# Kernel tuning notes

Measured on AMD Instinct MI355X. Metric: run time of the kernel, lower is better.

## Reference

```python
import jax, jax.numpy as jnp
import numpy as np


def _gcn_conv(x, src, dst, deg_inv_sqrt, W, b):
    # PyG GCNConv: h = x @ W; out = sum_{j->i} norm_ij * h_j  (+ bias)
    # src/dst already include self-loops; deg_inv_sqrt computed with self-loops.
    h = x @ W                                   # [N, F_out]
    norm = deg_inv_sqrt[src] * deg_inv_sqrt[dst]  # [E']
    msgs = h[src] * norm[:, None]               # [E', F_out] gather + scale
    out = jax.ops.segment_sum(msgs, dst, num_segments=x.shape[0])
    return out + b


def setup_inputs() -> dict:
    key = jax.random.key(0)
    k1, k2, k3, k4, k5 = jax.random.split(key, 5)
    N, E = 100000, 3200000
    in_c, hid, out_c = 256, 32, 128
    x = jax.random.normal(k1, (N, in_c), dtype=jnp.float32)
    edge_index = jax.random.randint(k2, (2, E), 0, N, dtype=jnp.int64)
    # Glorot-init weights, zero bias (PyG GCNConv defaults)
    W1 = jax.random.normal(k3, (in_c, hid), dtype=jnp.float32) * (2.0 / (in_c + hid)) ** 0.5
    b1 = jnp.zeros((hid,), dtype=jnp.float32)
    W2 = jax.random.normal(k4, (hid, out_c), dtype=jnp.float32) * (2.0 / (hid + out_c)) ** 0.5
    b2 = jnp.zeros((out_c,), dtype=jnp.float32)
    return {"x": x, "edge_index": edge_index, "W1": W1, "b1": b1, "W2": W2, "b2": b2}


def reference(x, edge_index, W1, b1, W2, b2):
    N = x.shape[0]
    # Add self-loops once; shared by both layers.
    loop = jnp.arange(N, dtype=edge_index.dtype)
    src = jnp.concatenate([edge_index[0], loop])
    dst = jnp.concatenate([edge_index[1], loop])
    deg = jax.ops.segment_sum(jnp.ones_like(dst, dtype=x.dtype), dst, num_segments=N)
    deg_inv_sqrt = jnp.where(deg > 0, jax.lax.rsqrt(deg), 0.0)

    h = _gcn_conv(x, src, dst, deg_inv_sqrt, W1, b1)
    h = jax.nn.relu(h)
    out = _gcn_conv(h, src, dst, deg_inv_sqrt, W2, b2)
    return out
```

## Files before the change

### kernel.cpp

```cpp
#include <hip/hip_runtime.h>

#define BSH 7
#define BNODES 128
#define SCHUNK 8192
#define MAXBUCK 800
#define G1_PAD 36

static __device__ __forceinline__ float frelu(float v){ return v > 0.f ? v : 0.f; }

__global__ void detect_kernel(const unsigned int* __restrict__ e, int* __restrict__ flag){
    __shared__ int odd_nz;
    if (threadIdx.x == 0) odd_nz = 0;
    __syncthreads();
    int local = 0;
    for (int i = threadIdx.x; i < 512; i += blockDim.x){
        if (e[2*i + 1] != 0u) local = 1;
    }
    if (local) atomicOr(&odd_nz, 1);
    __syncthreads();
    if (threadIdx.x == 0) *flag = (odd_nz == 0) ? 1 : 0;
}

static __device__ __forceinline__ int load_idx(const void* eidx, int flg, long long pos){
    if (flg) return (int)((const long long*)eidx)[pos];
    return ((const int*)eidx)[pos];
}

__global__ __launch_bounds__(512) void buckcount_kernel(const void* __restrict__ eidx,
        const int* __restrict__ flag, int* __restrict__ bcnt, int E, int nbuck){
    __shared__ int h[MAXBUCK];
    int tid = threadIdx.x;
    int flg = *flag;
    for (int i = tid; i < nbuck; i += 512) h[i] = 0;
    __syncthreads();
    long long c0 = (long long)blockIdx.x * SCHUNK;
    int cnt = (int)min((long long)SCHUNK, (long long)E - c0);
    for (int i = tid; i < cnt; i += 512)
        atomicAdd(&h[load_idx(eidx, flg, (long long)E + c0 + i) >> BSH], 1);
    __syncthreads();
    for (int i = tid; i < nbuck; i += 512)
        if (h[i]) atomicAdd(&bcnt[i], h[i]);
}

__global__ void bucket_scan_kernel(const int* __restrict__ bcnt, int* __restrict__ boff,
                                   int* __restrict__ bcursor, int nbuck){
    __shared__ int sums[1024];
    int tid = threadIdx.x;
    int s = (tid < nbuck) ? bcnt[tid] : 0;
    sums[tid] = s;
    __syncthreads();
    for (int off = 1; off < 1024; off <<= 1){
        int t = (tid >= off) ? sums[tid - off] : 0;
        __syncthreads();
        sums[tid] += t;
        __syncthreads();
    }
    if (tid < nbuck){
        int pfx = sums[tid] - s;
        boff[tid]    = pfx;
        bcursor[tid] = pfx;
    }
    if (tid == 0) boff[nbuck] = sums[1023];
}

__global__ __launch_bounds__(512) void binned_scatter_kernel(
        const void* __restrict__ eidx, const int* __restrict__ flag,
        int* __restrict__ bcursor, unsigned int* __restrict__ bpk, int E, int nbuck){
    __shared__ int hist[MAXBUCK];
    __shared__ int base[MAXBUCK];
    __shared__ unsigned short rank[SCHUNK];
    int tid = threadIdx.x;
    int flg = *flag;
    long long c0 = (long long)blockIdx.x * SCHUNK;
    int cnt = (int)min((long long)SCHUNK, (long long)E - c0);
    for (int i = tid; i < nbuck; i += 512) hist[i] = 0;
    __syncthreads();
    for (int i = tid; i < cnt; i += 512){
        int dst = load_idx(eidx, flg, (long long)E + c0 + i);
        rank[i] = (unsigned short)atomicAdd(&hist[dst >> BSH], 1);
    }
    __syncthreads();
    for (int i = tid; i < nbuck; i += 512){
        int h = hist[i];
        base[i] = h ? atomicAdd(&bcursor[i], h) : 0;
    }
    __syncthreads();
    for (int i = tid; i < cnt; i += 512){
        int src = load_idx(eidx, flg, c0 + i);
        int dst = load_idx(eidx, flg, (long long)E + c0 + i);
        unsigned int local = (unsigned int)(dst & (BNODES - 1));
        bpk[base[dst >> BSH] + (int)rank[i]] = (local << 24) | (unsigned int)src;
    }
}

__global__ __launch_bounds__(256) void node_sort_kernel(
        const unsigned int* __restrict__ bpk, const int* __restrict__ boff,
        int* __restrict__ csr, int* __restrict__ noff, int* __restrict__ deg,
        int N, int E, int nbuck){
    __shared__ int ndeg[BNODES];
    __shared__ int nbase[BNODES];
    __shared__ int ncur[BNODES];
    int b = blockIdx.x, tid = threadIdx.x;
    int beg = boff[b], end = boff[b + 1], len = end - beg;
    int nodeBase = b << BSH;
    int nNodes = min(BNODES, N - nodeBase);
    for (int i = tid; i < BNODES; i += 256) ndeg[i] = 0;
    __syncthreads();
    for (int i = tid; i < len; i += 256)
        atomicAdd(&ndeg[bpk[beg + i] >> 24], 1);
    __syncthreads();
    if (tid == 0){
        int r = beg;
        for (int l = 0; l < BNODES; ++l){ nbase[l] = r; ncur[l] = r; r += ndeg[l]; }
    }
    __syncthreads();
    for (int i = tid; i < nNodes; i += 256){
        deg[nodeBase + i]  = ndeg[i];
        noff[nodeBase + i] = nbase[i];
    }
    if (b == nbuck - 1 && tid == 0) noff[N] = E;
    for (int i = tid; i < len; i += 256){
        unsigned int p = bpk[beg + i];
        int pos = atomicAdd(&ncur[p >> 24], 1);
        csr[pos] = (int)(p & 0xFFFFFFu);
    }
}

__global__ void dis_kernel(const int* __restrict__ deg, float* __restrict__ dis, int N){
    int i = blockIdx.x * blockDim.x + threadIdx.x;
    if (i < N) dis[i] = rsqrtf((float)(deg[i] + 1));
}

__global__ __launch_bounds__(256) void gemm1_kernel(const float* __restrict__ x,
        const float* __restrict__ W1, const float* __restrict__ dis,
        float* __restrict__ h1s, int N){
    __shared__ float part[4][32][G1_PAD];
    int tid  = threadIdx.x;
    int lane = tid & 63;
    int wave = tid >> 6;
    int ty   = lane >> 3;
    int tx   = lane & 7;
    int rowT = blockIdx.x * 32 + ty * 4;

    const float4* xr[4];
#pragma unroll
    for (int r = 0; r < 4; ++r)
        xr[r] = (const float4*)(x + (size_t)min(rowT + r, N - 1) * 256) + wave * 16;
    const float4* wb = (const float4*)W1 + tx;

    float acc[4][4];
#pragma unroll
    for (int r = 0; r < 4; ++r)
#pragma unroll
        for (int c = 0; c < 4; ++c) acc[r][c] = 0.f;

#pragma unroll 4
    for (int kc = 0; kc < 16; ++kc){
        int kg = wave * 16 + kc;
        float4 xv[4], wv[4];
#pragma unroll
        for (int r = 0; r < 4; ++r) xv[r] = xr[r][kc];
#pragma unroll
        for (int k = 0; k < 4; ++k) wv[k] = wb[(kg * 4 + k) * 8];
#pragma unroll
        for (int r = 0; r < 4; ++r){
            acc[r][0] += xv[r].x*wv[0].x + xv[r].y*wv[1].x + xv[r].z*wv[2].x + xv[r].w*wv[3].x;
            acc[r][1] += xv[r].x*wv[0].y + xv[r].y*wv[1].y + xv[r].z*wv[2].y + xv[r].w*wv[3].y;
            acc[r][2] += xv[r].x*wv[0].z + xv[r].y*wv[1].z + xv[r].z*wv[2].z + xv[r].w*wv[3].z;
            acc[r][3] += xv[r].x*wv[0].w + xv[r].y*wv[1].w + xv[r].z*wv[2].w + xv[r].w*wv[3].w;
        }
    }

#pragma unroll
    for (int r = 0; r < 4; ++r)
        *(float4*)&part[wave][ty * 4 + r][tx * 4] =
            make_float4(acc[r][0], acc[r][1], acc[r][2], acc[r][3]);
    __syncthreads();

    int row = tid >> 3;
    int cq  = tid & 7;
    int grow = blockIdx.x * 32 + row;
    if (grow < N){
        float4 o = make_float4(0.f, 0.f, 0.f, 0.f);
#pragma unroll
        for (int w = 0; w < 4; ++w){
            float4 p = *(const float4*)&part[w][row][cq * 4];
            o.x += p.x; o.y += p.y; o.z += p.z; o.w += p.w;
        }
        float d = dis[grow];
        o.x *= d; o.y *= d; o.z *= d; o.w *= d;
        *(float4*)(h1s + (size_t)grow * 32 + cq * 4) = o;
    }
}

__global__ __launch_bounds__(256) void agg_kernel(
        const float* __restrict__ hs, const int* __restrict__ csr,
        const int* __restrict__ noff, const float* __restrict__ dis,
        const float* __restrict__ bias, float* __restrict__ outb,
        int N, int mode){
    int tid = threadIdx.x;
    int g   = blockIdx.x * 32 + (tid >> 3);
    int fq  = tid & 7;
    if (g >= N) return;
    const float4* hs4 = (const float4*)hs;
    int beg = noff[g], end = noff[g + 1];
    float4 acc = hs4[(size_t)g * 8 + fq];
    for (int k = beg; k < end; k += 8){
        int idxv = csr[k + fq];
#pragma unroll
        for (int u = 0; u < 8; ++u){
            int s = __shfl(idxv, u, 8);
            float4 v = hs4[(size_t)s * 8 + fq];
            float m = (k + u < end) ? 1.f : 0.f;
            acc.x += v.x * m; acc.y += v.y * m;
            acc.z += v.z * m; acc.w += v.w * m;
        }
    }
    float d = dis[g];
    float4 r;
    r.x = acc.x * d; r.y = acc.y * d; r.z = acc.z * d; r.w = acc.w * d;
    if (mode == 1){
        float4 bb = ((const float4*)bias)[fq];
        r.x = frelu(r.x + bb.x) * d; r.y = frelu(r.y + bb.y) * d;
        r.z = frelu(r.z + bb.z) * d; r.w = frelu(r.w + bb.w) * d;
    }
    ((float4*)outb)[(size_t)g * 8 + fq] = r;
}

__global__ __launch_bounds__(256) void gemm2_kernel(const float* __restrict__ a2,
        const float* __restrict__ W2, const float* __restrict__ b2,
        float* __restrict__ out, int N){
    int tid  = threadIdx.x;
    int colq = tid & 31;
    int rs   = tid >> 5;
    int rowT = blockIdx.x * 16 + rs * 2;

    const float4* ar[2];
#pragma unroll
    for (int r = 0; r < 2; ++r)
        ar[r] = (const float4*)(a2 + (size_t)min(rowT + r, N - 1) * 32);
    const float4* wq = (const float4*)W2 + colq;

    float acc[2][4];
#pragma unroll
    for (int r = 0; r < 2; ++r)
#pragma unroll
        for (int c = 0; c < 4; ++c) acc[r][c] = 0.f;

#pragma unroll
    for (int kc = 0; kc < 8; ++kc){
        float4 av[2], wv[4];
#pragma unroll
        for (int r = 0; r < 2; ++r) av[r] = ar[r][kc];
#pragma unroll
        for (int k = 0; k < 4; ++k) wv[k] = wq[(kc * 4 + k) * 32];
#pragma unroll
        for (int r = 0; r < 2; ++r){
            acc[r][0] += av[r].x*wv[0].x + av[r].y*wv[1].x + av[r].z*wv[2].x + av[r].w*wv[3].x;
            acc[r][1] += av[r].x*wv[0].y + av[r].y*wv[1].y + av[r].z*wv[2].y + av[r].w*wv[3].y;
            acc[r][2] += av[r].x*wv[0].z + av[r].y*wv[1].z + av[r].z*wv[2].z + av[r].w*wv[3].z;
            acc[r][3] += av[r].x*wv[0].w + av[r].y*wv[1].w + av[r].z*wv[2].w + av[r].w*wv[3].w;
        }
    }
    float4 bb = ((const float4*)b2)[colq];
#pragma unroll
    for (int r = 0; r < 2; ++r){
        int row = rowT + r;
        if (row < N){
            float4 o = make_float4(acc[r][0] + bb.x, acc[r][1] + bb.y,
                                   acc[r][2] + bb.z, acc[r][3] + bb.w);
            *(float4*)(out + (size_t)row * 128 + colq * 4) = o;
        }
    }
}

extern "C" void kernel_launch(void* const* d_in, const int* in_sizes, int n_in,
                              void* d_out, int out_size, void* d_ws, size_t ws_size,
                              hipStream_t stream){
    const float* x  = (const float*)d_in[0];
    const void*  ei = d_in[1];
    const float* W1 = (const float*)d_in[2];
    const float* b1 = (const float*)d_in[3];
    const float* W2 = (const float*)d_in[4];
    const float* b2 = (const float*)d_in[5];
    float* out = (float*)d_out;

    const int N = in_sizes[0] / 256;
    const int E = in_sizes[1] / 2;
    const int nbuck = (N + BNODES - 1) >> BSH;

    char* ws = (char*)d_ws;
    size_t off = 0;
    auto alloc = [&](size_t bytes) -> char* {
        char* p = ws + off;
        off = (off + bytes + 255) & ~(size_t)255;
        return p;
    };
    int*   flag    = (int*)  alloc(4);
    int*   bcnt    = (int*)  alloc((size_t)nbuck * 4);
    int*   boff    = (int*)  alloc((size_t)(nbuck + 1) * 4);
    int*   bcursor = (int*)  alloc((size_t)nbuck * 4);
    int*   deg     = (int*)  alloc((size_t)N * 4);
    int*   noff    = (int*)  alloc((size_t)(N + 1) * 4);
    float* dis     = (float*)alloc((size_t)N * 4);
    unsigned int* bpk = (unsigned int*)alloc((size_t)E * 4);
    int*   csr     = (int*)  alloc((size_t)(E + 8) * 4);
    float* h1s     = (float*)alloc((size_t)N * 32 * 4);
    float* h2s     = (float*)alloc((size_t)N * 32 * 4);
    float* a2      = h1s;

    hipMemsetAsync(bcnt, 0, (size_t)nbuck * 4, stream);
    hipMemsetAsync(csr + E, 0, 8 * 4, stream);

    const int nchunk = (E + SCHUNK - 1) / SCHUNK;
    detect_kernel        <<<1, 256, 0, stream>>>((const unsigned int*)ei, flag);
    buckcount_kernel     <<<nchunk, 512, 0, stream>>>(ei, flag, bcnt, E, nbuck);
    bucket_scan_kernel   <<<1, 1024, 0, stream>>>(bcnt, boff, bcursor, nbuck);
    binned_scatter_kernel<<<nchunk, 512, 0, stream>>>(ei, flag, bcursor, bpk, E, nbuck);
    node_sort_kernel     <<<nbuck, 256, 0, stream>>>(bpk, boff, csr, noff, deg, N, E, nbuck);
    dis_kernel           <<<(N + 255) / 256, 256, 0, stream>>>(deg, dis, N);

    gemm1_kernel <<<(N + 31) / 32, 256, 0, stream>>>(x, W1, dis, h1s, N);
    agg_kernel   <<<(N + 31) / 32, 256, 0, stream>>>(h1s, csr, noff, dis, b1, h2s, N, 1);
    agg_kernel   <<<(N + 31) / 32, 256, 0, stream>>>(h2s, csr, noff, dis, b2, a2, N, 0);
    gemm2_kernel <<<(N + 15) / 16, 256, 0, stream>>>(a2, W2, b2, out, N);
}
```

Baseline: 303.9 us.

## Stage x tile into LDS via global_load_lds in gemm1 and drop split-K reduction

The first-layer GEMM now copies each block's 32x256 tile of x straight into padded shared memory using the direct global-to-LDS load builtin, then each thread computes one row by four output columns over the full K. This replaces the earlier per-wave split-K scheme, which read x directly from global memory and needed a shared-memory partial reduction. The aim is coalesced, asynchronous streaming of x without going through registers, and no reduction step. In exchange each thread has fewer accumulators, so there is less register-level reuse of W1, and about 33KB of LDS per block may limit occupancy.

```diff
diff --git a/kernel.cpp b/kernel.cpp
--- a/kernel.cpp
+++ b/kernel.cpp
@@ -4,9 +4,12 @@
 #define BNODES 128
 #define SCHUNK 8192
 #define MAXBUCK 800
-#define G1_PAD 36
+#define XS_STRIDE 260
 
 static __device__ __forceinline__ float frelu(float v){ return v > 0.f ? v : 0.f; }
+
+typedef __attribute__((address_space(1))) const void gas_t;
+typedef __attribute__((address_space(3))) void las_t;
 
 __global__ void detect_kernel(const unsigned int* __restrict__ e, int* __restrict__ flag){
     __shared__ int odd_nz;
@@ -134,62 +137,47 @@
 __global__ __launch_bounds__(256) void gemm1_kernel(const float* __restrict__ x,
         const float* __restrict__ W1, const float* __restrict__ dis,
         float* __restrict__ h1s, int N){
-    __shared__ float part[4][32][G1_PAD];
-    int tid  = threadIdx.x;
+    __shared__ float xs[32 * XS_STRIDE];
+    int tid = threadIdx.x;
+    int rowBase = blockIdx.x * 32;
+#pragma unroll
+    for (int i = 0; i < 8; ++i){
+        int q     = i * 256 + tid;
+        int row   = q >> 6;
+        int chunk = q & 63;
+        int grow  = min(rowBase + row, N - 1);
+        const float* src = x + (size_t)grow * 256 + chunk * 4;
+        __builtin_amdgcn_global_load_lds((gas_t*)src,
+            (las_t*)&xs[row * XS_STRIDE + chunk * 4], 16, 0, 0);
+    }
+    __syncthreads();
+
     int lane = tid & 63;
     int wave = tid >> 6;
     int ty   = lane >> 3;
     int tx   = lane & 7;
-    int rowT = blockIdx.x * 32 + ty * 4;
-
-    const float4* xr[4];
-#pragma unroll
-    for (int r = 0; r < 4; ++r)
-        xr[r] = (const float4*)(x + (size_t)min(rowT + r, N - 1) * 256) + wave * 16;
-    const float4* wb = (const float4*)W1 + tx;
-
-    float acc[4][4];
-#pragma unroll
-    for (int r = 0; r < 4; ++r)
-#pragma unroll
-        for (int c = 0; c < 4; ++c) acc[r][c] = 0.f;
-
+    int rowL = wave * 8 + ty;
+    const float4* xrow = (const float4*)&xs[rowL * XS_STRIDE];
+    const float4* wb   = (const float4*)W1 + tx;
+
+    float a0 = 0.f, a1 = 0.f, a2 = 0.f, a3 = 0.f;
 #pragma unroll 4
-    for (int kc = 0; kc < 16; ++kc){
-        int kg = wave * 16 + kc;
-        float4 xv[4], wv[4];
-#pragma unroll
-        for (int r = 0; r < 4; ++r) xv[r] = xr[r][kc];
-#pragma unroll
-        for (int k = 0; k < 4; ++k) wv[k] = wb[(kg * 4 + k) * 8];
-#pragma unroll
-        for (int r = 0; r < 4; ++r){
-            acc[r][0] += xv[r].x*wv[0].x + xv[r].y*wv[1].x + xv[r].z*wv[2].x + xv[r].w*wv[3].x;
-            acc[r][1] += xv[r].x*wv[0].y + xv[r].y*wv[1].y + xv[r].z*wv[2].y + xv[r].w*wv[3].y;
-            acc[r][2] += xv[r].x*wv[0].z + xv[r].y*wv[1].z + xv[r].z*wv[2].z + xv[r].w*wv[3].z;
-            acc[r][3] += xv[r].x*wv[0].w + xv[r].y*wv[1].w + xv[r].z*wv[2].w + xv[r].w*wv[3].w;
-        }
-    }
-
-#pragma unroll
-    for (int r = 0; r < 4; ++r)
-        *(float4*)&part[wave][ty * 4 + r][tx * 4] =
-            make_float4(acc[r][0], acc[r][1], acc[r][2], acc[r][3]);
-    __syncthreads();
-
-    int row = tid >> 3;
-    int cq  = tid & 7;
-    int grow = blockIdx.x * 32 + row;
+    for (int kc = 0; kc < 64; ++kc){
+        float4 xv  = xrow[kc];
+        float4 wv0 = wb[(kc * 4 + 0) * 8];
+        float4 wv1 = wb[(kc * 4 + 1) * 8];
+        float4 wv2 = wb[(kc * 4 + 2) * 8];
+        float4 wv3 = wb[(kc * 4 + 3) * 8];
+        a0 += xv.x*wv0.x + xv.y*wv1.x + xv.z*wv2.x + xv.w*wv3.x;
+        a1 += xv.x*wv0.y + xv.y*wv1.y + xv.z*wv2.y + xv.w*wv3.y;
+        a2 += xv.x*wv0.z + xv.y*wv1.z + xv.z*wv2.z + xv.w*wv3.z;
+        a3 += xv.x*wv0.w + xv.y*wv1.w + xv.z*wv2.w + xv.w*wv3.w;
+    }
+    int grow = rowBase + rowL;
     if (grow < N){
-        float4 o = make_float4(0.f, 0.f, 0.f, 0.f);
-#pragma unroll
-        for (int w = 0; w < 4; ++w){
-            float4 p = *(const float4*)&part[w][row][cq * 4];
-            o.x += p.x; o.y += p.y; o.z += p.z; o.w += p.w;
-        }
         float d = dis[grow];
-        o.x *= d; o.y *= d; o.z *= d; o.w *= d;
-        *(float4*)(h1s + (size_t)grow * 32 + cq * 4) = o;
+        *(float4*)(h1s + (size_t)grow * 32 + tx * 4) =
+            make_float4(a0 * d, a1 * d, a2 * d, a3 * d);
     }
 }
 
```

Result: slower. 343.6 us (+13.1%).
